# Performance work log

Measured on AMD Instinct MI355X. Metric: run time of the kernel, lower is better.

Reference implementation:

```python
import jax, jax.numpy as jnp
import numpy as np

N, E = 10000, 160000          # nodes, edges
MUL = 128                     # channel multiplicity of 0e and 1o blocks
NSP = 10                      # node_attrs (species one-hot) dim
NRAD = 8                      # edge_feats radial basis dim
SILU_C = 1.6790               # e3nn normalize2mom constant for SiLU
AVG_NEIGH = 16.0
SQ3 = np.sqrt(3.0).astype(np.float32)


def setup_inputs() -> dict:
    key = jax.random.key(0)
    ks = jax.random.split(key, 14)
    d = {}
    d["node_feats"] = jax.random.normal(ks[0], (N, 4 * MUL), jnp.float32)   # [N, 128 + 128*3]
    d["node_attrs"] = jax.random.normal(ks[1], (N, NSP), jnp.float32)
    d["edge_feats"] = jax.random.normal(ks[2], (E, NRAD), jnp.float32)
    d["edge_attrs"] = jax.random.normal(ks[3], (E, 4), jnp.float32)          # [0e | 1o]
    d["edge_index"] = jax.random.randint(ks[4], (2, E), 0, N, jnp.int32)
    # e3nn internal weights are standard normal; normalization applied in forward
    d["lin1_ws"] = jax.random.normal(ks[5], (MUL, MUL), jnp.float32)
    d["lin1_wv"] = jax.random.normal(ks[6], (MUL, MUL), jnp.float32)
    d["fc_w0"] = jax.random.normal(ks[7], (NRAD, 64), jnp.float32)
    d["fc_w1"] = jax.random.normal(ks[8], (64, 64), jnp.float32)
    d["fc_w2"] = jax.random.normal(ks[9], (64, 4 * MUL), jnp.float32)        # tp.weight_numel = 512
    d["lin2_ws"] = jax.random.normal(ks[10], (2 * MUL, MUL), jnp.float32)    # 256x0e -> 128x0e
    d["lin2_wv"] = jax.random.normal(ks[11], (2 * MUL, MUL), jnp.float32)    # 256x1o -> 128x1o
    d["sc_ws"] = jax.random.normal(ks[12], (MUL, NSP, MUL), jnp.float32)
    d["sc_wv"] = jax.random.normal(ks[13], (MUL, NSP, MUL), jnp.float32)
    return d


def _fc(ef, w0, w1, w2):
    # e3nn FullyConnectedNet: x @ W / sqrt(fan_in), normalize2mom-scaled SiLU between layers
    h = SILU_C * jax.nn.silu(ef @ w0 / np.float32(np.sqrt(NRAD)))
    h = SILU_C * jax.nn.silu(h @ w1 / np.float32(8.0))
    return h @ w2 / np.float32(8.0)


def reference(node_feats, node_attrs, edge_feats, edge_attrs, edge_index,
              lin1_ws, lin1_wv, fc_w0, fc_w1, fc_w2,
              lin2_ws, lin2_wv, sc_ws, sc_wv):
    x_s = node_feats[:, :MUL]                       # [N, 128] scalar block
    x_v = node_feats[:, MUL:].reshape(N, MUL, 3)    # [N, 128, 3] vector block

    # self-connection: FullyConnectedTensorProduct with 10x0e attrs; path weight 1/sqrt(mul1*mul2)
    sc_norm = np.float32(1.0 / np.sqrt(MUL * NSP))
    sc_s = jnp.einsum('nu,nv,uvw->nw', x_s, node_attrs, sc_ws) * sc_norm
    sc_v = jnp.einsum('nuc,nv,uvw->nwc', x_v, node_attrs, sc_wv) * sc_norm

    # linear_1 (per-irrep channel mixing, fan_in = 128)
    l1 = np.float32(1.0 / np.sqrt(MUL))
    y_s = (x_s @ lin1_ws) * l1
    y_v = jnp.einsum('nuc,uw->nwc', x_v, lin1_wv) * l1

    src = edge_index[1]
    dst = edge_index[0]
    xs_e = y_s[src]                                 # [E, 128]
    xv_e = y_v[src]                                 # [E, 128, 3]
    a_s = edge_attrs[:, :1]                         # [E, 1]
    a_v = edge_attrs[:, 1:]                         # [E, 3]

    w = _fc(edge_feats, fc_w0, fc_w1, fc_w2)        # [E, 512]
    w_ss, w_sv, w_vs, w_vv = jnp.split(w, 4, axis=1)  # instruction order in source

    # 'uvu' weighted tensor product with e3nn component/element normalization:
    # net coefficient per path works out to 1 except 1o x 1o -> 0e which is 1/sqrt(3)
    mid_s0 = w_ss * xs_e * a_s                                          # 0e*0e->0e
    mid_s1 = w_vv * jnp.einsum('euc,ec->eu', xv_e, a_v) / SQ3           # 1o*1o->0e
    mid_v2 = (w_sv * xs_e)[:, :, None] * a_v[:, None, :]                # 0e*1o->1o
    mid_v3 = w_vs[:, :, None] * xv_e * a_s[:, :, None]                  # 1o*0e->1o

    inv = np.float32(1.0 / np.sqrt(AVG_NEIGH))
    s = jax.ops.segment_sum(jnp.concatenate([mid_s0, mid_s1], axis=1), dst, num_segments=N) * inv  # [N, 256]
    v = jax.ops.segment_sum(jnp.concatenate([mid_v2, mid_v3], axis=1), dst, num_segments=N) * inv  # [N, 256, 3]

    # linear_2 (fan_in = 256)
    l2 = np.float32(1.0 / np.sqrt(2 * MUL))
    out_s = (s @ lin2_ws) * l2 + sc_s
    out_v = jnp.einsum('nuc,uw->nwc', v, lin2_wv) * l2 + sc_v

    return jnp.concatenate([out_s, out_v.reshape(N, 3 * MUL)], axis=1)   # [N, 512]
```

## Files before the change

kernel.cpp:

```cpp
#include <hip/hip_runtime.h>
#include <hip/hip_bf16.h>
#include <math.h>

#define N_NODES 10000
#define N_EDGES 160000
#define S_BLK 79
#define V_BLK 235

typedef __attribute__((ext_vector_type(8))) short short8x;
typedef __attribute__((ext_vector_type(4))) float floatx4;
typedef __attribute__((ext_vector_type(4))) unsigned int uint4x;
typedef __attribute__((ext_vector_type(2))) unsigned int uint2x;

union S8 { short8x v; unsigned short u[8]; uint4 q; };
union U2 { uint2x v; unsigned short us[4]; };

__device__ __forceinline__ unsigned short f2bf(float x) {
    unsigned int u = __float_as_uint(x);
    return (unsigned short)((u + 0x7fffu + ((u >> 16) & 1u)) >> 16);
}
__device__ __forceinline__ float bf2f(unsigned short u) {
    return __uint_as_float(((unsigned)u) << 16);
}
__device__ __forceinline__ float silu_c(float x) {
    return 1.679f * x / (1.0f + __expf(-x));
}

__global__ __launch_bounds__(256) void pack_all_kernel(
    const float* __restrict__ sc_ws, const float* __restrict__ lin2_ws,
    const float* __restrict__ sc_wv, const float* __restrict__ lin2_wv,
    const float* __restrict__ fc_w2, const float* __restrict__ fc_w1,
    const float* __restrict__ lin1_ws, const float* __restrict__ lin1_wv,
    unsigned short* __restrict__ b_pre, unsigned short* __restrict__ w2a,
    unsigned short* __restrict__ w1a, unsigned short* __restrict__ b_lin)
{
    const int bid = blockIdx.x;
    const int t = threadIdx.x;
    if (bid < 192) {
        int id = bid * 256 + t;
        int mat = id / 24576;
        int slot = id - mat * 24576;
        int ks = slot >> 9;
        int rr = slot & 511;
        int lane = rr & 63;
        int quad = lane >> 4;
        int n = ((rr >> 6) << 4) + (lane & 15);
        const float* sc  = mat ? sc_wv  : sc_ws;
        const float* lin = mat ? lin2_wv : lin2_ws;
        S8 pk;
        #pragma unroll
        for (int j = 0; j < 8; j++) {
            int k = ks * 32 + quad * 8 + j;
            float w;
            if (k < 1280) {
                int u = k & 127, v = k >> 7;
                w = sc[(u * 10 + v) * 128 + n];
            } else {
                w = lin[(k - 1280) * 128 + n];
            }
            pk.u[j] = f2bf(w);
        }
        *(uint4*)(b_pre + (size_t)id * 8) = pk.q;
    } else if (bid < 208) {
        int id = (bid - 192) * 256 + t;
        int lane = id & 63;
        int mfg = (id >> 6) & 31;
        int ks = id >> 11;
        int col = mfg * 16 + (lane & 15);
        int k0 = ks * 32 + (lane >> 4) * 8;
        S8 pk;
        #pragma unroll
        for (int j = 0; j < 8; j++)
            pk.u[j] = f2bf(fc_w2[(k0 + j) * 512 + col] * 0.125f);
        *(uint4*)(w2a + (size_t)id * 8) = pk.q;
    } else if (bid < 210) {
        int id = (bid - 208) * 256 + t;
        int lane = id & 63;
        int mf = (id >> 6) & 3;
        int ks = id >> 8;
        int m = mf * 16 + (lane & 15);
        int k0 = ks * 32 + (lane >> 4) * 8;
        S8 pk;
        #pragma unroll
        for (int j = 0; j < 8; j++)
            pk.u[j] = f2bf(fc_w1[(k0 + j) * 64 + m] * 0.125f);
        *(uint4*)(w1a + (size_t)id * 8) = pk.q;
    } else {
        int id = (bid - 210) * 256 + t;
        int mat = id >> 11;
        int slot = id & 2047;
        int ks = slot >> 9;
        int rr = slot & 511;
        int nf = rr >> 6;
        int lane = rr & 63;
        int n = nf * 16 + (lane & 15);
        int k0 = ks * 32 + (lane >> 4) * 8;
        const float* w = mat ? lin1_wv : lin1_ws;
        const float l1 = 0.0883883476483f;
        S8 pk;
        #pragma unroll
        for (int j = 0; j < 8; j++)
            pk.u[j] = f2bf(w[(k0 + j) * 128 + n] * l1);
        *(uint4*)(b_lin + (size_t)id * 8) = pk.q;
    }
}

__global__ __launch_bounds__(256) void node_lin1_mfma(
    const float* __restrict__ node_feats,
    const unsigned short* __restrict__ b_lin,
    unsigned short* __restrict__ y_pk,
    unsigned short* __restrict__ xvP16)
{
    __shared__ __align__(16) unsigned char smem[32768];
    short8x* Al = (short8x*)smem;
    unsigned short* Yt = (unsigned short*)smem;

    const int blk = blockIdx.x;
    const int t = threadIdx.x;
    const int base = blk * 32;
    const int lane = t & 63;
    const int wv = t >> 6;
    const int m15 = lane & 15;
    const int k0q = (lane >> 4) * 8;

    #pragma unroll
    for (int it = 0; it < 8; it++) {
        int g = wv * 8 + it;
        int af = g >> 2;
        int ks = g & 3;
        int m = af * 16 + m15;
        int comp = m >> 5;
        int nloc = m & 31;
        int node = base + nloc;
        int valid = (node < N_NODES);
        if (!valid) node = N_NODES - 1;
        int k0 = ks * 32 + k0q;
        const float* row = node_feats + (size_t)node * 512;
        S8 pk;
        if (comp == 0) {
            float4 a = *(const float4*)&row[k0];
            float4 b = *(const float4*)&row[k0 + 4];
            pk.u[0] = f2bf(a.x); pk.u[1] = f2bf(a.y); pk.u[2] = f2bf(a.z); pk.u[3] = f2bf(a.w);
            pk.u[4] = f2bf(b.x); pk.u[5] = f2bf(b.y); pk.u[6] = f2bf(b.z); pk.u[7] = f2bf(b.w);
        } else {
            int c = comp - 1;
            #pragma unroll
            for (int j = 0; j < 8; j++)
                pk.u[j] = f2bf(row[128 + (k0 + j) * 3 + c]);
            if (valid)
                *(uint4*)&xvP16[((size_t)node * 3 + c) * 128 + k0] = pk.q;
        }
        Al[(ks * 8 + af) * 64 + lane] = pk.v;
    }
    __syncthreads();

    floatx4 c[8][2];
    #pragma unroll
    for (int af = 0; af < 8; af++) {
        c[af][0] = (floatx4){0.f, 0.f, 0.f, 0.f};
        c[af][1] = (floatx4){0.f, 0.f, 0.f, 0.f};
    }

    const uint4* bq = (const uint4*)b_lin;
    #pragma unroll
    for (int ks = 0; ks < 4; ks++) {
        S8 bs0, bs1, bv0, bv1;
        bs0.q = bq[       ks*512 + (wv*2+0)*64 + lane];
        bs1.q = bq[       ks*512 + (wv*2+1)*64 + lane];
        bv0.q = bq[2048 + ks*512 + (wv*2+0)*64 + lane];
        bv1.q = bq[2048 + ks*512 + (wv*2+1)*64 + lane];
        #pragma unroll
        for (int af = 0; af < 8; af++) {
            short8x a = Al[(ks*8 + af)*64 + lane];
            if (af < 2) {
                c[af][0] = __builtin_amdgcn_mfma_f32_16x16x32_bf16(a, bs0.v, c[af][0], 0, 0, 0);
                c[af][1] = __builtin_amdgcn_mfma_f32_16x16x32_bf16(a, bs1.v, c[af][1], 0, 0, 0);
            } else {
                c[af][0] = __builtin_amdgcn_mfma_f32_16x16x32_bf16(a, bv0.v, c[af][0], 0, 0, 0);
                c[af][1] = __builtin_amdgcn_mfma_f32_16x16x32_bf16(a, bv1.v, c[af][1], 0, 0, 0);
            }
        }
    }
    __syncthreads();

    {
        const int rq = (lane >> 4) * 4;
        #pragma unroll
        for (int af = 0; af < 8; af++) {
            #pragma unroll
            for (int nf = 0; nf < 2; nf++) {
                int u = wv * 32 + nf * 16 + m15;
                #pragma unroll
                for (int i = 0; i < 4; i++) {
                    int m = af * 16 + rq + i;
                    int comp = m >> 5, nloc = m & 31;
                    Yt[(nloc * 128 + u) * 4 + comp] = f2bf(c[af][nf][i]);
                }
            }
        }
    }
    __syncthreads();
    {
        unsigned short* dst = y_pk + (size_t)base * 512;
        int nrem = N_NODES - base;
        #pragma unroll
        for (int it = 0; it < 8; it++) {
            int idx = it * 256 + t;
            if ((idx >> 6) < nrem)
                *(uint4*)(dst + (size_t)idx * 8) = *(const uint4*)&Yt[idx * 8];
        }
    }
}

__global__ __launch_bounds__(256) void hist_kernel(const int* __restrict__ edge_index,
                                                   int* __restrict__ deg) {
    int e = blockIdx.x * 256 + threadIdx.x;
    if (e < N_EDGES) atomicAdd(&deg[edge_index[e]], 1);
}

__global__ __launch_bounds__(1024) void scan_kernel(const int* __restrict__ deg,
                                                    int* __restrict__ row_start,
                                                    int* __restrict__ cursor) {
    __shared__ int wsum[16];
    __shared__ int carry_s;
    const int t = threadIdx.x;
    const int lane = t & 63, w = t >> 6;
    if (t == 0) carry_s = 0;
    __syncthreads();
    for (int chunk = 0; chunk < 10; chunk++) {
        int idx = chunk * 1024 + t;
        int v = (idx < N_NODES) ? deg[idx] : 0;
        int x = v;
        #pragma unroll
        for (int off = 1; off < 64; off <<= 1) {
            int yv = __shfl_up(x, off, 64);
            if (lane >= off) x += yv;
        }
        if (lane == 63) wsum[w] = x;
        __syncthreads();
        int wpre = 0;
        for (int i = 0; i < w; i++) wpre += wsum[i];
        int incl = x + wpre + carry_s;
        int excl = incl - v;
        if (idx < N_NODES) { row_start[idx] = excl; cursor[idx] = excl; }
        __syncthreads();
        if (t == 1023) carry_s = incl;
        __syncthreads();
    }
    if (t == 0) row_start[N_NODES] = carry_s;
}

__global__ __launch_bounds__(256) void scatter_kernel(const int* __restrict__ edge_index,
                                                      const float* __restrict__ edge_attrs,
                                                      int* __restrict__ cursor,
                                                      int* __restrict__ edge_list,
                                                      int* __restrict__ srcs,
                                                      float* __restrict__ ea_sorted) {
    int e = blockIdx.x * 256 + threadIdx.x;
    if (e < N_EDGES) {
        int pos = atomicAdd(&cursor[edge_index[e]], 1);
        edge_list[pos] = e;
        srcs[pos] = edge_index[N_EDGES + e];
        float4 ea = *(const float4*)(edge_attrs + (size_t)e * 4);
        *(float4*)(ea_sorted + (size_t)pos * 4) = ea;
    }
}

__global__ __launch_bounds__(256) void edge_w_mfma(
    const float* __restrict__ edge_feats,
    const int* __restrict__ edge_list,
    const float* __restrict__ fc_w0,
    const unsigned short* __restrict__ w1a,
    const unsigned short* __restrict__ w2a,
    unsigned short* __restrict__ w_pk)
{
    __shared__ __align__(16) unsigned char smem[26368];
    float* ef = (float*)smem;
    unsigned short* h0b = (unsigned short*)(smem + 2304);
    unsigned short* T   = (unsigned short*)smem;
    unsigned short* h1b = (unsigned short*)(smem + 16896);
    int* eids = (int*)(smem + 26112);

    const int blk = blockIdx.x;
    const int t = threadIdx.x;
    const int eb0 = blk * 64;
    const int lane = t & 63;
    const int wv = t >> 6;
    const int quad = lane >> 4;
    const int m15 = lane & 15;

    if (t < 64) eids[t] = edge_list[eb0 + t];
    __syncthreads();

    #pragma unroll
    for (int r = 0; r < 2; r++) {
        int idx = r * 256 + t;
        int el = idx >> 3;
        int k = idx & 7;
        ef[el * 9 + k] = edge_feats[(size_t)eids[el] * 8 + k];
    }
    __syncthreads();

    {
        const int e_loc = t >> 2;
        const int c0 = (t & 3) * 16;
        float a0[16];
        #pragma unroll
        for (int i = 0; i < 16; i++) a0[i] = 0.f;
        const float* efr = &ef[e_loc * 9];
        #pragma unroll
        for (int k = 0; k < 8; k++) {
            float ek = efr[k];
            float w[16];
            #pragma unroll
            for (int q4 = 0; q4 < 4; q4++)
                *(float4*)&w[q4*4] = *(const float4*)&fc_w0[k*64 + c0 + q4*4];
            #pragma unroll
            for (int i = 0; i < 16; i++) a0[i] += ek * w[i];
        }
        const float is8 = 0.35355339059f;
        S8 p0, p1;
        #pragma unroll
        for (int i = 0; i < 8; i++) {
            p0.u[i] = f2bf(silu_c(a0[i] * is8));
            p1.u[i] = f2bf(silu_c(a0[8 + i] * is8));
        }
        *(uint4*)&h0b[e_loc * 72 + c0]     = p0.q;
        *(uint4*)&h0b[e_loc * 72 + c0 + 8] = p1.q;
    }
    __syncthreads();

    {
        floatx4 c2[4];
        #pragma unroll
        for (int ee = 0; ee < 4; ee++) c2[ee] = (floatx4){0.f, 0.f, 0.f, 0.f};
        const uint4* w1aq = (const uint4*)w1a;
        #pragma unroll
        for (int ks = 0; ks < 2; ks++) {
            S8 afr;
            afr.q = w1aq[(ks*4 + wv)*64 + lane];
            #pragma unroll
            for (int ee = 0; ee < 4; ee++) {
                S8 bfr;
                bfr.q = *(const uint4*)&h0b[(ee*16 + m15) * 72 + ks*32 + quad*8];
                c2[ee] = __builtin_amdgcn_mfma_f32_16x16x32_bf16(afr.v, bfr.v, c2[ee], 0, 0, 0);
            }
        }
        #pragma unroll
        for (int ee = 0; ee < 4; ee++) {
            ushort4 pk = make_ushort4(f2bf(silu_c(c2[ee][0])), f2bf(silu_c(c2[ee][1])),
                                      f2bf(silu_c(c2[ee][2])), f2bf(silu_c(c2[ee][3])));
            *(ushort4*)&h1b[(ee*16 + m15) * 72 + wv*16 + quad*4] = pk;
        }
    }
    __syncthreads();

    const uint4* w2aq = (const uint4*)w2a;
    #pragma unroll 1
    for (int p = 0; p < 4; p++) {
        floatx4 c3[2][4];
        #pragma unroll
        for (int mf = 0; mf < 2; mf++)
            #pragma unroll
            for (int ee = 0; ee < 4; ee++)
                c3[mf][ee] = (floatx4){0.f, 0.f, 0.f, 0.f};

        #pragma unroll
        for (int ks = 0; ks < 2; ks++) {
            S8 bfr[4];
            #pragma unroll
            for (int ee = 0; ee < 4; ee++)
                bfr[ee].q = *(const uint4*)&h1b[(ee*16 + m15) * 72 + ks*32 + quad*8];
            #pragma unroll
            for (int mf = 0; mf < 2; mf++) {
                S8 afr;
                afr.q = w2aq[(size_t)(ks*32 + wv*8 + p*2 + mf) * 64 + lane];
                #pragma unroll
                for (int ee = 0; ee < 4; ee++)
                    c3[mf][ee] = __builtin_amdgcn_mfma_f32_16x16x32_bf16(afr.v, bfr[ee].v, c3[mf][ee], 0, 0, 0);
            }
        }

        __syncthreads();
        #pragma unroll
        for (int mf = 0; mf < 2; mf++) {
            #pragma unroll
            for (int ee = 0; ee < 4; ee++) {
                int e = ee*16 + m15;
                #pragma unroll
                for (int i = 0; i < 4; i++) {
                    int colp = mf*16 + quad*4 + i;
                    T[e*132 + colp*4 + wv] = f2bf(c3[mf][ee][i]);
                }
            }
        }
        __syncthreads();

        #pragma unroll
        for (int it = 0; it < 8; it++) {
            int idx = it * 256 + t;
            int e  = idx >> 5;
            int cu = idx & 31;
            uint2x v = *(const uint2x*)&T[e*132 + cu*4];
            unsigned short* dstp = w_pk + ((size_t)(eb0 + e) * 128 + p*32 + cu) * 4;
            __builtin_nontemporal_store(v, (uint2x*)dstp);
        }
    }
}

__global__ __launch_bounds__(256) void gather_kernel(
    const int* __restrict__ row_start,
    const int* __restrict__ srcs,
    const float* __restrict__ ea_sorted,
    const unsigned short* __restrict__ w_pk,
    const unsigned short* __restrict__ y_pk,
    float* __restrict__ accS,
    float* __restrict__ accV)
{
    const int t = threadIdx.x;
    const int half = t >> 7;
    const int u = t & 127;
    const int n = blockIdx.x * 2 + half;
    const int sbeg = row_start[n];
    const int send = row_start[n + 1];

    float aS0 = 0.f, aS1 = 0.f;
    float aV2x = 0.f, aV2y = 0.f, aV2z = 0.f;
    float aV3x = 0.f, aV3y = 0.f, aV3z = 0.f;

    U2 wq_n; ushort4 yq_n; float4 ea_n;
    wq_n.v = (uint2x){0u, 0u};
    yq_n = make_ushort4(0, 0, 0, 0);
    ea_n = make_float4(0.f, 0.f, 0.f, 0.f);
    if (sbeg < send) {
        wq_n.v = __builtin_nontemporal_load((const uint2x*)(w_pk + ((size_t)sbeg * 128 + u) * 4));
        int s0 = srcs[sbeg];
        yq_n = *(const ushort4*)(y_pk + ((size_t)s0 * 128 + u) * 4);
        ea_n = *(const float4*)(ea_sorted + (size_t)sbeg * 4);
    }
    for (int i = sbeg; i < send; i++) {
        U2 wq = wq_n; ushort4 yq = yq_n; float4 ea = ea_n;
        int inx = i + 1;
        if (inx < send) {
            wq_n.v = __builtin_nontemporal_load((const uint2x*)(w_pk + ((size_t)inx * 128 + u) * 4));
            int s1 = srcs[inx];
            yq_n = *(const ushort4*)(y_pk + ((size_t)s1 * 128 + u) * 4);
            ea_n = *(const float4*)(ea_sorted + (size_t)inx * 4);
        }
        float wss = bf2f(wq.us[0]), wsv = bf2f(wq.us[1]);
        float wvs = bf2f(wq.us[2]), wvv = bf2f(wq.us[3]);
        float qs = bf2f(yq.x), q0 = bf2f(yq.y), q1 = bf2f(yq.z), q2 = bf2f(yq.w);
        aS0 += wss * qs * ea.x;
        aS1 += wvv * (q0*ea.y + q1*ea.z + q2*ea.w);
        float tsv = wsv * qs;
        aV2x += tsv * ea.y; aV2y += tsv * ea.z; aV2z += tsv * ea.w;
        float tvs = wvs * ea.x;
        aV3x += tvs * q0; aV3y += tvs * q1; aV3z += tvs * q2;
    }

    const float inv = 0.25f;
    const float s1c = 0.57735026919f * 0.25f;
    accS[(size_t)n * 256 + u]       = aS0 * inv;
    accS[(size_t)n * 256 + 128 + u] = aS1 * s1c;
    float* av0 = accV + ((size_t)n * 3 + 0) * 256;
    float* av1 = accV + ((size_t)n * 3 + 1) * 256;
    float* av2 = accV + ((size_t)n * 3 + 2) * 256;
    av0[u] = aV2x * inv;  av0[128 + u] = aV3x * inv;
    av1[u] = aV2y * inv;  av1[128 + u] = aV3y * inv;
    av2[u] = aV2z * inv;  av2[128 + u] = aV3z * inv;
}

__global__ __launch_bounds__(256) void node_out_mfma(
    const float* __restrict__ node_feats,
    const float* __restrict__ node_attrs,
    const unsigned short* __restrict__ xvP16,
    const float* __restrict__ accS,
    const float* __restrict__ accV,
    const unsigned short* __restrict__ b_pre,
    float* __restrict__ out)
{
    __shared__ short8x Al[512];
    const int bid = blockIdx.x;
    const int t = threadIdx.x;
    const int lane = t & 63;
    const int wv = t >> 6;
    const bool is_s = (bid < S_BLK);

    const int r0g = t >> 2;
    const int q = t & 3;
    const float* pxA[2];
    const unsigned short* pxvA[2];
    const float* paA[2];
    const float* patA[2];
    #pragma unroll
    for (int j = 0; j < 2; j++) {
        int r = r0g + j * 64;
        if (is_s) {
            int R = bid * 128 + r;
            int node = (R < N_NODES) ? R : 0;
            pxA[j]  = node_feats + (size_t)node * 512;
            pxvA[j] = nullptr;
            paA[j]  = accS + (size_t)node * 256;
            patA[j] = node_attrs + node * 10;
        } else {
            int Rg = (bid - S_BLK) * 128 + r;
            if (Rg >= 3 * N_NODES) Rg = 0;
            int node = Rg / 3;
            pxA[j]  = nullptr;
            pxvA[j] = xvP16 + (size_t)Rg * 128;
            paA[j]  = accV + (size_t)Rg * 256;
            patA[j] = node_attrs + node * 10;
        }
    }
    int aslot[2];
    #pragma unroll
    for (int j = 0; j < 2; j++) {
        int r = r0g + j * 64;
        aslot[j] = ((r >> 4) << 6) + (q << 4) + (r & 15);
    }

    const uint4* bfrag_base = (const uint4*)(b_pre) + (is_s ? 0 : 24576);
    const float sc_norm = 0.02795084972f;
    const float l2 = 0.0625f;

    floatx4 c[8][2];
    #pragma unroll
    for (int af = 0; af < 8; af++) {
        c[af][0] = (floatx4){0.f, 0.f, 0.f, 0.f};
        c[af][1] = (floatx4){0.f, 0.f, 0.f, 0.f};
    }

    for (int ks = 0; ks < 48; ks++) {
        S8 b0, b1;
        b0.q = bfrag_base[ks*512 + (wv*2+0)*64 + lane];
        b1.q = bfrag_base[ks*512 + (wv*2+1)*64 + lane];

        __syncthreads();
        {
            int k0 = ks * 32 + q * 8;
            #pragma unroll
            for (int j = 0; j < 2; j++) {
                S8 pk;
                if (k0 < 1280) {
                    int u0 = k0 & 127;
                    float att = patA[j][k0 >> 7] * sc_norm;
                    if (is_s) {
                        #pragma unroll
                        for (int i = 0; i < 8; i++)
                            pk.u[i] = f2bf(pxA[j][u0 + i] * att);
                    } else {
                        #pragma unroll
                        for (int i = 0; i < 8; i++)
                            pk.u[i] = f2bf(bf2f(pxvA[j][u0 + i]) * att);
                    }
                } else {
                    int j2 = k0 - 1280;
                    #pragma unroll
                    for (int i = 0; i < 8; i++)
                        pk.u[i] = f2bf(paA[j][j2 + i] * l2);
                }
                Al[aslot[j]] = pk.v;
            }
        }
        __syncthreads();

        #pragma unroll
        for (int af = 0; af < 8; af++) {
            short8x a = Al[af*64 + lane];
            c[af][0] = __builtin_amdgcn_mfma_f32_16x16x32_bf16(a, b0.v, c[af][0], 0, 0, 0);
            c[af][1] = __builtin_amdgcn_mfma_f32_16x16x32_bf16(a, b1.v, c[af][1], 0, 0, 0);
        }
    }

    const int m = lane & 15;
    const int rq = (lane >> 4) * 4;
    if (is_s) {
        const int n0 = bid * 128;
        #pragma unroll
        for (int af = 0; af < 8; af++) {
            #pragma unroll
            for (int i = 0; i < 4; i++) {
                int n = n0 + af*16 + rq + i;
                if (n < N_NODES) {
                    out[(size_t)n*512 + wv*32 + m]      = c[af][0][i];
                    out[(size_t)n*512 + wv*32 + 16 + m] = c[af][1][i];
                }
            }
        }
    } else {
        const int r0 = (bid - S_BLK) * 128;
        #pragma unroll
        for (int af = 0; af < 8; af++) {
            #pragma unroll
            for (int i = 0; i < 4; i++) {
                int Rg = r0 + af*16 + rq + i;
                if (Rg < 3 * N_NODES) {
                    int nn = Rg / 3;
                    int cc = Rg - nn * 3;
                    float* po = out + (size_t)nn*512 + 128 + cc;
                    po[(wv*32 + m)*3]      = c[af][0][i];
                    po[(wv*32 + 16 + m)*3] = c[af][1][i];
                }
            }
        }
    }
}

extern "C" void kernel_launch(void* const* d_in, const int* in_sizes, int n_in,
                              void* d_out, int out_size, void* d_ws, size_t ws_size,
                              hipStream_t stream) {
    const float* node_feats = (const float*)d_in[0];
    const float* node_attrs = (const float*)d_in[1];
    const float* edge_feats = (const float*)d_in[2];
    const float* edge_attrs = (const float*)d_in[3];
    const int*   edge_index = (const int*)  d_in[4];
    const float* lin1_ws    = (const float*)d_in[5];
    const float* lin1_wv    = (const float*)d_in[6];
    const float* fc_w0      = (const float*)d_in[7];
    const float* fc_w1      = (const float*)d_in[8];
    const float* fc_w2      = (const float*)d_in[9];
    const float* lin2_ws    = (const float*)d_in[10];
    const float* lin2_wv    = (const float*)d_in[11];
    const float* sc_ws      = (const float*)d_in[12];
    const float* sc_wv      = (const float*)d_in[13];
    float* out = (float*)d_out;

    unsigned short* y_pk  = (unsigned short*)d_ws;
    float* accS = (float*)(y_pk + (size_t)5120000);
    float* accV = accS + (size_t)2560000;
    unsigned short* xvP16 = (unsigned short*)(accV + (size_t)7680000);
    unsigned short* w_pk  = xvP16 + (size_t)3840000;
    int* deg       = (int*)(w_pk + (size_t)81920000);
    int* row_start = deg + 10016;
    int* cursor    = row_start + 10016;
    int* edge_list = cursor + 10016;
    int* srcs      = edge_list + N_EDGES;
    float* ea_sorted = (float*)(srcs + N_EDGES);
    unsigned short* b_pre = (unsigned short*)(ea_sorted + (size_t)N_EDGES * 4);
    unsigned short* w2a   = b_pre + (size_t)2 * 24576 * 8;
    unsigned short* w1a   = w2a + (size_t)4096 * 8;
    unsigned short* b_lin = w1a + (size_t)512 * 8;
    const size_t need = (size_t)5120000 * 2 + (size_t)(2560000 + 7680000) * 4
                      + (size_t)3840000 * 2 + (size_t)81920000 * 2
                      + (size_t)(10016 * 3 + N_EDGES * 2) * 4
                      + (size_t)N_EDGES * 4 * 4
                      + ((size_t)2 * 24576 * 8 + (size_t)4096 * 8 + (size_t)512 * 8
                         + (size_t)4096 * 8) * 2;
    if (ws_size < need) return;

    hipLaunchKernelGGL(pack_all_kernel, dim3(226), dim3(256), 0, stream,
                       sc_ws, lin2_ws, sc_wv, lin2_wv, fc_w2, fc_w1, lin1_ws, lin1_wv,
                       b_pre, w2a, w1a, b_lin);
    hipLaunchKernelGGL(node_lin1_mfma, dim3(313), dim3(256), 0, stream,
                       node_feats, b_lin, y_pk, xvP16);

    hipMemsetAsync(deg, 0, (size_t)N_NODES * sizeof(int), stream);
    hipLaunchKernelGGL(hist_kernel, dim3(625), dim3(256), 0, stream, edge_index, deg);
    hipLaunchKernelGGL(scan_kernel, dim3(1), dim3(1024), 0, stream, deg, row_start, cursor);
    hipLaunchKernelGGL(scatter_kernel, dim3(625), dim3(256), 0, stream,
                       edge_index, edge_attrs, cursor, edge_list, srcs, ea_sorted);
    hipLaunchKernelGGL(edge_w_mfma, dim3(2500), dim3(256), 0, stream,
                       edge_feats, edge_list, fc_w0, w1a, w2a, w_pk);
    hipLaunchKernelGGL(gather_kernel, dim3(5000), dim3(256), 0, stream,
                       row_start, srcs, ea_sorted, w_pk, y_pk, accS, accV);

    hipLaunchKernelGGL(node_out_mfma, dim3(S_BLK + V_BLK), dim3(256), 0, stream,
                       node_feats, node_attrs, xvP16, accS, accV, b_pre, out);
}
```

Measured before the change: 340.3 us.

## Split each node's edge gather across two half-blocks with deeper prefetch

```diff
diff --git a/kernel.cpp b/kernel.cpp
--- a/kernel.cpp
+++ b/kernel.cpp
@@ -417,10 +417,11 @@
     float* __restrict__ accS,
     float* __restrict__ accV)
 {
+    __shared__ float sm[2][128][9];
     const int t = threadIdx.x;
-    const int half = t >> 7;
+    const int h = t >> 7;
     const int u = t & 127;
-    const int n = blockIdx.x * 2 + half;
+    const int n = blockIdx.x;
     const int sbeg = row_start[n];
     const int send = row_start[n + 1];
 
@@ -428,46 +429,95 @@
     float aV2x = 0.f, aV2y = 0.f, aV2z = 0.f;
     float aV3x = 0.f, aV3y = 0.f, aV3z = 0.f;
 
-    U2 wq_n; ushort4 yq_n; float4 ea_n;
-    wq_n.v = (uint2x){0u, 0u};
-    yq_n = make_ushort4(0, 0, 0, 0);
-    ea_n = make_float4(0.f, 0.f, 0.f, 0.f);
     if (sbeg < send) {
-        wq_n.v = __builtin_nontemporal_load((const uint2x*)(w_pk + ((size_t)sbeg * 128 + u) * 4));
-        int s0 = srcs[sbeg];
-        yq_n = *(const ushort4*)(y_pk + ((size_t)s0 * 128 + u) * 4);
-        ea_n = *(const float4*)(ea_sorted + (size_t)sbeg * 4);
-    }
-    for (int i = sbeg; i < send; i++) {
-        U2 wq = wq_n; ushort4 yq = yq_n; float4 ea = ea_n;
-        int inx = i + 1;
-        if (inx < send) {
-            wq_n.v = __builtin_nontemporal_load((const uint2x*)(w_pk + ((size_t)inx * 128 + u) * 4));
-            int s1 = srcs[inx];
-            yq_n = *(const ushort4*)(y_pk + ((size_t)s1 * 128 + u) * 4);
-            ea_n = *(const float4*)(ea_sorted + (size_t)inx * 4);
-        }
-        float wss = bf2f(wq.us[0]), wsv = bf2f(wq.us[1]);
-        float wvs = bf2f(wq.us[2]), wvv = bf2f(wq.us[3]);
-        float qs = bf2f(yq.x), q0 = bf2f(yq.y), q1 = bf2f(yq.z), q2 = bf2f(yq.w);
-        aS0 += wss * qs * ea.x;
-        aS1 += wvv * (q0*ea.y + q1*ea.z + q2*ea.w);
-        float tsv = wsv * qs;
-        aV2x += tsv * ea.y; aV2y += tsv * ea.z; aV2z += tsv * ea.w;
-        float tvs = wvs * ea.x;
-        aV3x += tvs * q0; aV3y += tvs * q1; aV3z += tvs * q2;
-    }
+        const int last = send - 1;
+        const int i0 = sbeg + h;
+
+        int j0 = (i0     < send) ? i0     : last;
+        int j1 = (i0 + 2 < send) ? i0 + 2 : last;
+        int s0 = srcs[j0];
+        int s1 = srcs[j1];
+
+        U2 wqA, wqB; ushort4 yqA, yqB; float4 eaA, eaB;
+        wqA.v = __builtin_nontemporal_load((const uint2x*)(w_pk + ((size_t)j0 * 128 + u) * 4));
+        eaA   = *(const float4*)(ea_sorted + (size_t)j0 * 4);
+        yqA   = *(const ushort4*)(y_pk + ((size_t)s0 * 128 + u) * 4);
+        wqB.v = __builtin_nontemporal_load((const uint2x*)(w_pk + ((size_t)j1 * 128 + u) * 4));
+        eaB   = *(const float4*)(ea_sorted + (size_t)j1 * 4);
+        yqB   = *(const ushort4*)(y_pk + ((size_t)s1 * 128 + u) * 4);
+
+        int sP0 = srcs[(i0 + 4 < send) ? i0 + 4 : last];
+        int sP1 = srcs[(i0 + 6 < send) ? i0 + 6 : last];
+
+        for (int i = i0; i < send; i += 4) {
+            {
+                float wss = bf2f(wqA.us[0]), wsv = bf2f(wqA.us[1]);
+                float wvs = bf2f(wqA.us[2]), wvv = bf2f(wqA.us[3]);
+                float qs = bf2f(yqA.x), q0 = bf2f(yqA.y), q1 = bf2f(yqA.z), q2 = bf2f(yqA.w);
+                aS0 += wss * qs * eaA.x;
+                aS1 += wvv * (q0*eaA.y + q1*eaA.z + q2*eaA.w);
+                float tsv = wsv * qs;
+                aV2x += tsv * eaA.y; aV2y += tsv * eaA.z; aV2z += tsv * eaA.w;
+                float tvs = wvs * eaA.x;
+                aV3x += tvs * q0; aV3y += tvs * q1; aV3z += tvs * q2;
+            }
+            {
+                int jn = (i + 4 < send) ? i + 4 : last;
+                wqA.v = __builtin_nontemporal_load((const uint2x*)(w_pk + ((size_t)jn * 128 + u) * 4));
+                eaA   = *(const float4*)(ea_sorted + (size_t)jn * 4);
+                yqA   = *(const ushort4*)(y_pk + ((size_t)sP0 * 128 + u) * 4);
+                sP0 = srcs[(i + 8 < send) ? i + 8 : last];
+            }
+            {
+                float m = (i + 2 < send) ? 1.f : 0.f;
+                float ex = eaB.x * m, ey = eaB.y * m, ez = eaB.z * m, ew = eaB.w * m;
+                float wss = bf2f(wqB.us[0]), wsv = bf2f(wqB.us[1]);
+                float wvs = bf2f(wqB.us[2]), wvv = bf2f(wqB.us[3]);
+                float qs = bf2f(yqB.x), q0 = bf2f(yqB.y), q1 = bf2f(yqB.z), q2 = bf2f(yqB.w);
+                aS0 += wss * qs * ex;
+                aS1 += wvv * (q0*ey + q1*ez + q2*ew);
+                float tsv = wsv * qs;
+                aV2x += tsv * ey; aV2y += tsv * ez; aV2z += tsv * ew;
+                float tvs = wvs * ex;
+                aV3x += tvs * q0; aV3y += tvs * q1; aV3z += tvs * q2;
+            }
+            {
+                int jn = (i + 6 < send) ? i + 6 : last;
+                wqB.v = __builtin_nontemporal_load((const uint2x*)(w_pk + ((size_t)jn * 128 + u) * 4));
+                eaB   = *(const float4*)(ea_sorted + (size_t)jn * 4);
+                yqB   = *(const ushort4*)(y_pk + ((size_t)sP1 * 128 + u) * 4);
+                sP1 = srcs[(i + 10 < send) ? i + 10 : last];
+            }
+        }
+    }
+
+    sm[h][u][0] = aS0;  sm[h][u][1] = aS1;
+    sm[h][u][2] = aV2x; sm[h][u][3] = aV2y;
+    sm[h][u][4] = aV2z; sm[h][u][5] = aV3x;
+    sm[h][u][6] = aV3y; sm[h][u][7] = aV3z;
+    __syncthreads();
 
     const float inv = 0.25f;
     const float s1c = 0.57735026919f * 0.25f;
-    accS[(size_t)n * 256 + u]       = aS0 * inv;
-    accS[(size_t)n * 256 + 128 + u] = aS1 * s1c;
-    float* av0 = accV + ((size_t)n * 3 + 0) * 256;
-    float* av1 = accV + ((size_t)n * 3 + 1) * 256;
-    float* av2 = accV + ((size_t)n * 3 + 2) * 256;
-    av0[u] = aV2x * inv;  av0[128 + u] = aV3x * inv;
-    av1[u] = aV2y * inv;  av1[128 + u] = aV3y * inv;
-    av2[u] = aV2z * inv;  av2[128 + u] = aV3z * inv;
+    if (h == 0) {
+        float v0 = sm[0][u][0] + sm[1][u][0];
+        float v1 = sm[0][u][1] + sm[1][u][1];
+        float v2 = sm[0][u][2] + sm[1][u][2];
+        float v3 = sm[0][u][3] + sm[1][u][3];
+        accS[(size_t)n * 256 + u]       = v0 * inv;
+        accS[(size_t)n * 256 + 128 + u] = v1 * s1c;
+        accV[((size_t)n * 3 + 0) * 256 + u] = v2 * inv;
+        accV[((size_t)n * 3 + 1) * 256 + u] = v3 * inv;
+    } else {
+        float v4 = sm[0][u][4] + sm[1][u][4];
+        float v5 = sm[0][u][5] + sm[1][u][5];
+        float v6 = sm[0][u][6] + sm[1][u][6];
+        float v7 = sm[0][u][7] + sm[1][u][7];
+        accV[((size_t)n * 3 + 2) * 256 + u]       = v4 * inv;
+        accV[((size_t)n * 3 + 0) * 256 + 128 + u] = v5 * inv;
+        accV[((size_t)n * 3 + 1) * 256 + 128 + u] = v6 * inv;
+        accV[((size_t)n * 3 + 2) * 256 + 128 + u] = v7 * inv;
+    }
 }
 
 __global__ __launch_bounds__(256) void node_out_mfma(
@@ -661,7 +711,7 @@
                        edge_index, edge_attrs, cursor, edge_list, srcs, ea_sorted);
     hipLaunchKernelGGL(edge_w_mfma, dim3(2500), dim3(256), 0, stream,
                        edge_feats, edge_list, fc_w0, w1a, w2a, w_pk);
-    hipLaunchKernelGGL(gather_kernel, dim3(5000), dim3(256), 0, stream,
+    hipLaunchKernelGGL(gather_kernel, dim3(N_NODES), dim3(256), 0, stream,
                        row_start, srcs, ea_sorted, w_pk, y_pk, accS, accV);
 
     hipLaunchKernelGGL(node_out_mfma, dim3(S_BLK + V_BLK), dim3(256), 0, stream,
```

Result: faster. 320.6 us (-5.8%).
